# Optimization experiments

Hardware: AMD Instinct MI355X
Metric: run time of the kernel (lower is better)

The kernel has to match this reference:

```python
import jax, jax.numpy as jnp
import numpy as np
from jax import lax

KSIZE = 7
EPS = 1e-10


def _circular_mask(k=KSIZE):
    # faithful to EdgeLoss.cal_mask: inclusive circle, normalized by count
    xs = np.arange(k, dtype=np.float32)
    d2 = (xs[:, None] + 0.5 - k / 2) ** 2 + (xs[None, :] + 0.5 - k / 2) ** 2
    m = (d2 <= ((k - 1) / 2) ** 2).astype(np.float32)
    return jnp.asarray(m / m.sum())


def _gather_logp(prob, target):
    # prob: (B,C,H,W), target: (B,H,W) int -> log prob at target class, (B,1,H,W)
    logpt = jnp.log(prob + EPS)
    return jnp.take_along_axis(logpt, target[:, None, :, :], axis=1)


def _focal0(prob, target):
    # FocalLoss(gamma=0, alpha=None): mean of -log p_t
    return jnp.mean(-_gather_logp(prob, target))


def _dice(prob, target):
    t = target.astype(prob.dtype)          # (B,H,W)
    p = prob[:, 1, :, :]                   # foreground channel
    I = jnp.sum(p * t, axis=(1, 2))
    U = jnp.sum(p + t, axis=(1, 2))
    return 1.0 - jnp.mean(2.0 * I / (U + EPS))


def _edge(prob, target, mask):
    # circular box-filter average of target == unfold+mask sum (zero padding)
    t = target.astype(prob.dtype)[:, None, :, :]  # (B,1,H,W)
    ave = lax.conv_general_dilated(t, mask[None, None, :, :], (1, 1), 'SAME')
    at = jnp.abs(t - ave)                          # edge weight (B,1,H,W)
    lp = _gather_logp(prob, target)                # (B,1,H,W)
    return jnp.mean(-lp * at)


def _calloss(prob, target, sigmas, mask):
    return (_focal0(prob, target) / sigmas[0]
            + _dice(prob, target) / sigmas[1]
            + _edge(prob, target, mask) / sigmas[2])


def setup_inputs() -> dict:
    key = jax.random.key(0)
    k1, k2, k3, k4, k5 = jax.random.split(key, 5)
    N, M, B, C, H, W = 2, 1, 8, 2, 1024, 1024
    predictions = jax.random.normal(k1, (N, B, C, H, W), dtype=jnp.float32)
    Diss = jax.random.uniform(k2, (M, B, C, H, W), dtype=jnp.float32)
    target = jax.random.randint(k3, (B, H, W), 0, 2, dtype=jnp.int32)
    diff = jax.random.normal(k4, (), dtype=jnp.float32)
    sigma = jax.random.uniform(k5, (3,), dtype=jnp.float32, minval=0.5, maxval=1.5)
    return {"predictions": predictions, "Diss": Diss, "target": target,
            "diff": diff, "sigma": sigma}


def reference(predictions, Diss, target, diff, sigma):
    mask = _circular_mask()
    sigmas = sigma * sigma
    loss = jnp.asarray(0.0, dtype=predictions.dtype)
    for i in range(predictions.shape[0]):            # deep-supervision heads
        prob = jax.nn.softmax(predictions[i], axis=1)
        loss = loss + _calloss(prob, target, sigmas, mask)
    for j in range(Diss.shape[0]):                   # already-probabilities
        loss = loss + _calloss(Diss[j], target, sigmas, mask)
    loss = loss + diff                               # len(diff) != 0 branch
    loss = loss + jnp.sum(jnp.log(sigmas)) / 2
    return loss
```

## Files before the change

kernel.cpp:

```cpp
#include <hip/hip_runtime.h>
#include <math.h>

#define BB 8
#define HH 1024
#define WW 1024
#define HW (1024*1024)

#define TW 128
#define TH 16
#define HALO_H (TH+6)
#define TSTRIDE 136
#define NCHUNK (HALO_H*34)
#define NCOPY 64
#define CSTRIDE 64
#define NSLOT 18

__device__ __forceinline__ void pin4(float4& v) {
    asm volatile("" : "+v"(v.x), "+v"(v.y), "+v"(v.z), "+v"(v.w));
}

__global__ __launch_bounds__(256, 4)
void loss_main(const float* __restrict__ pred,
               const float* __restrict__ diss,
               const int*   __restrict__ target,
               double*      __restrict__ acc)
{
    __shared__ __align__(16) unsigned char tile[HALO_H][TSTRIDE];
    __shared__ __align__(16) unsigned char h5[HALO_H][TW];
    __shared__ __align__(16) unsigned char h7[HALO_H][TW];
    __shared__ float red[4][12];

    const int bx = blockIdx.x;
    const int by = blockIdx.y;
    const int b  = blockIdx.z;
    const int x0 = bx * TW, y0 = by * TH;
    const int tid = threadIdx.x;
    const int txx = tid & 31;
    const int ty  = tid >> 5;

    const float* p00 = pred + ((size_t)(0 * BB + b) * 2 + 0) * HW;
    const float* p01 = p00 + HW;
    const float* p10 = pred + ((size_t)(1 * BB + b) * 2 + 0) * HW;
    const float* p11 = p10 + HW;
    const float* q0  = diss + ((size_t)b * 2 + 0) * HW;
    const float* q1  = q0 + HW;

    const int x  = txx * 4;
    const int gx = x0 + x;
    const size_t offA = (size_t)(y0 + ty) * WW + gx;
    const size_t offB = offA + (size_t)8 * WW;

    float4 v00a = *(const float4*)(p00 + offA);
    float4 v01a = *(const float4*)(p01 + offA);
    float4 v10a = *(const float4*)(p10 + offA);
    float4 v11a = *(const float4*)(p11 + offA);
    float4 w0a  = *(const float4*)(q0  + offA);
    float4 w1a  = *(const float4*)(q1  + offA);
    float4 v00b = *(const float4*)(p00 + offB);
    float4 v01b = *(const float4*)(p01 + offB);
    float4 v10b = *(const float4*)(p10 + offB);
    float4 v11b = *(const float4*)(p11 + offB);
    float4 w0b  = *(const float4*)(q0  + offB);
    float4 w1b  = *(const float4*)(q1  + offB);
    __builtin_amdgcn_sched_barrier(0);

    const int* tgt_b = target + (size_t)b * HW;
    int4 iv[3]; int rr[3], mm[3];
    bool act[3], mainp[3], rowin[3];
    #pragma unroll
    for (int i = 0; i < 3; ++i) {
        const int ch = tid + 256 * i;
        const bool a = ch < NCHUNK;
        const int chc = a ? ch : 0;
        const int r = chc / 34;
        const int m = chc - r * 34;
        const int gy  = y0 - 3 + r;
        const int gxb = x0 - 4 + 4 * m;
        const bool ri = (gy >= 0) && (gy < HH);
        const bool fp = a && ri && (gxb >= 0) && (gxb + 3 < WW);
        act[i] = a; rr[i] = r; mm[i] = m; rowin[i] = ri; mainp[i] = fp;
        const int gyc  = ri ? gy  : 0;
        const int gxbc = fp ? gxb : 0;
        iv[i] = *(const int4*)(tgt_b + (size_t)gyc * WW + gxbc);
    }
    #pragma unroll
    for (int i = 0; i < 3; ++i) {
        if (!act[i]) continue;
        unsigned v = 0u;
        if (mainp[i]) {
            v = (unsigned)(iv[i].x & 0xff)
              | ((unsigned)(iv[i].y & 0xff) << 8)
              | ((unsigned)(iv[i].z & 0xff) << 16)
              | ((unsigned)(iv[i].w & 0xff) << 24);
        } else if (rowin[i]) {
            const int gy  = y0 - 3 + rr[i];
            const int gxb = x0 - 4 + 4 * mm[i];
            #pragma unroll
            for (int j = 0; j < 4; ++j) {
                const int gxj = gxb + j;
                if (gxj >= 0 && gxj < WW)
                    v |= (unsigned)(tgt_b[(size_t)gy * WW + gxj] & 0xff) << (8 * j);
            }
        }
        *(unsigned*)&tile[rr[i]][4 * mm[i]] = v;
    }

    pin4(v00a); pin4(v01a); pin4(v10a); pin4(v11a); pin4(w0a); pin4(w1a);
    pin4(v00b); pin4(v01b); pin4(v10b); pin4(v11b); pin4(w0b); pin4(w1b);
    __syncthreads();

    for (int g = tid; g < HALO_H * 32; g += 256) {
        int r  = g >> 5;
        int xg = (g & 31) << 2;
        unsigned c0 = *(const unsigned*)&tile[r][xg];
        unsigned c1 = *(const unsigned*)&tile[r][xg + 4];
        unsigned c2 = *(const unsigned*)&tile[r][xg + 8];
        unsigned A1 = (c0 >> 8)  | (c1 << 24);
        unsigned A2 = (c0 >> 16) | (c1 << 16);
        unsigned A3 = (c0 >> 24) | (c1 << 8);
        unsigned A5 = (c1 >> 8)  | (c2 << 24);
        unsigned A6 = (c1 >> 16) | (c2 << 16);
        unsigned A7 = (c1 >> 24) | (c2 << 8);
        unsigned v5 = A2 + A3 + c1 + A5 + A6;
        unsigned v7 = v5 + A1 + A7;
        *(unsigned*)&h5[r][xg] = v5;
        *(unsigned*)&h7[r][xg] = v7;
    }
    __syncthreads();

    float sf0=0.f, se0=0.f, si0=0.f, sp0=0.f;
    float sf1=0.f, se1=0.f, si1=0.f, sp1=0.f;
    float sf2=0.f, se2=0.f, si2=0.f, sd1=0.f;
    float st = 0.f;

    const unsigned t4a   = *(const unsigned*)&tile[ty + 3][x + 4];
    const unsigned cnt4a = *(const unsigned*)&tile[ty    ][x + 4]
                         + *(const unsigned*)&tile[ty + 6][x + 4]
                         + *(const unsigned*)&h5[ty + 1][x]
                         + *(const unsigned*)&h5[ty + 2][x]
                         + *(const unsigned*)&h7[ty + 3][x]
                         + *(const unsigned*)&h5[ty + 4][x]
                         + *(const unsigned*)&h5[ty + 5][x];
    const unsigned t4b   = *(const unsigned*)&tile[ty + 11][x + 4];
    const unsigned cnt4b = *(const unsigned*)&tile[ty +  8][x + 4]
                         + *(const unsigned*)&tile[ty + 14][x + 4]
                         + *(const unsigned*)&h5[ty +  9][x]
                         + *(const unsigned*)&h5[ty + 10][x]
                         + *(const unsigned*)&h7[ty + 11][x]
                         + *(const unsigned*)&h5[ty + 12][x]
                         + *(const unsigned*)&h5[ty + 13][x];

    auto half = [&](unsigned t4, unsigned cnt4,
                    const float4& v00, const float4& v01,
                    const float4& v10, const float4& v11,
                    const float4& w0,  const float4& w1) {
        #pragma unroll
        for (int j = 0; j < 4; ++j) {
            const unsigned tb = (t4 >> (8 * j)) & 0xffu;
            const float t  = (float)tb;
            const float at = fabsf(t - (float)((cnt4 >> (8 * j)) & 0xffu) * (1.0f / 29.0f));
            st += t;
            {
                float a0 = ((const float*)&v00)[j], a1 = ((const float*)&v01)[j];
                float p1v = __builtin_amdgcn_rcpf(1.0f + __expf(a0 - a1));
                float pt  = (tb != 0u) ? p1v : 1.0f - p1v;
                float lp  = __logf(pt + 1e-10f);
                sf0 -= lp; se0 -= lp * at; si0 += p1v * t; sp0 += p1v;
            }
            {
                float a0 = ((const float*)&v10)[j], a1 = ((const float*)&v11)[j];
                float p1v = __builtin_amdgcn_rcpf(1.0f + __expf(a0 - a1));
                float pt  = (tb != 0u) ? p1v : 1.0f - p1v;
                float lp  = __logf(pt + 1e-10f);
                sf1 -= lp; se1 -= lp * at; si1 += p1v * t; sp1 += p1v;
            }
            {
                float d0 = ((const float*)&w0)[j], d1 = ((const float*)&w1)[j];
                float pt = (tb != 0u) ? d1 : d0;
                float lp = __logf(pt + 1e-10f);
                sf2 -= lp; se2 -= lp * at; si2 += d1 * t; sd1 += d1;
            }
        }
    };
    half(t4a, cnt4a, v00a, v01a, v10a, v11a, w0a, w1a);
    half(t4b, cnt4b, v00b, v01b, v10b, v11b, w0b, w1b);

    float vals[12] = {sf0,se0,si0,sp0+st, sf1,se1,si1,sp1+st, sf2,se2,si2,sd1+st};
    #pragma unroll
    for (int j = 0; j < 12; ++j) {
        float v = vals[j];
        #pragma unroll
        for (int s = 32; s > 0; s >>= 1) v += __shfl_down(v, s, 64);
        vals[j] = v;
    }
    const int wave = tid >> 6;
    const int lane = tid & 63;
    if (lane == 0) {
        #pragma unroll
        for (int j = 0; j < 12; ++j) red[wave][j] = vals[j];
    }
    __syncthreads();
    if (tid < 12) {
        double s = (double)red[0][tid] + (double)red[1][tid]
                 + (double)red[2][tid] + (double)red[3][tid];
        const int img  = tid >> 2;
        const int what = tid & 3;
        int slot;
        if      (what == 0) slot = 0;
        else if (what == 1) slot = 1;
        else if (what == 2) slot = 2 + b;
        else                slot = 10 + b;
        const int copy = (by * 8 + bx) & (NCOPY - 1);
        unsafeAtomicAdd(acc + (size_t)copy * CSTRIDE + (img * NSLOT + slot), s);
    }
}

__global__ __launch_bounds__(256)
void finalize_kernel(const double* __restrict__ acc,
                     const float*  __restrict__ diff,
                     const float*  __restrict__ sigma,
                     float*        __restrict__ out)
{
    __shared__ double ssum[54];
    const int t = threadIdx.x;
    if (t < 216) {
        const int slot_lin = t >> 2;
        const int part     = t & 3;
        const double* p = acc + slot_lin + (size_t)part * 16 * CSTRIDE;
        double s = 0.0;
        #pragma unroll
        for (int j = 0; j < 16; ++j) s += p[(size_t)j * CSTRIDE];
        s += __shfl_down(s, 1, 64);
        s += __shfl_down(s, 2, 64);
        if (part == 0) ssum[slot_lin] = s;
    }
    __syncthreads();
    if (t == 0) {
        const double sig0 = (double)sigma[0] * (double)sigma[0];
        const double sig1 = (double)sigma[1] * (double)sigma[1];
        const double sig2 = (double)sigma[2] * (double)sigma[2];
        const double inv  = 1.0 / (double)((size_t)BB * HW);
        double loss = 0.0;
        for (int i = 0; i < 3; ++i) {
            const double* A = ssum + i * NSLOT;
            double focal = A[0] * inv;
            double edge  = A[1] * inv;
            double dsum  = 0.0;
            for (int b = 0; b < BB; ++b)
                dsum += 2.0 * A[2 + b] / (A[10 + b] + 1e-10);
            double dice = 1.0 - dsum / (double)BB;
            loss += focal / sig0 + dice / sig1 + edge / sig2;
        }
        loss += (double)diff[0];
        loss += 0.5 * (log(sig0) + log(sig1) + log(sig2));
        out[0] = (float)loss;
    }
}

extern "C" void kernel_launch(void* const* d_in, const int* in_sizes, int n_in,
                              void* d_out, int out_size, void* d_ws, size_t ws_size,
                              hipStream_t stream)
{
    const float* pred   = (const float*)d_in[0];
    const float* diss   = (const float*)d_in[1];
    const int*   target = (const int*)  d_in[2];
    const float* diff   = (const float*)d_in[3];
    const float* sigma  = (const float*)d_in[4];
    double* acc = (double*)d_ws;

    (void)hipMemsetAsync(d_ws, 0, (size_t)NCOPY * CSTRIDE * sizeof(double), stream);

    dim3 grid(WW / TW, HH / TH, BB);
    loss_main<<<grid, 256, 0, stream>>>(pred, diss, target, acc);
    finalize_kernel<<<1, 256, 0, stream>>>(acc, diff, sigma, (float*)d_out);
}
```

Measured before the change: 268.5 us.

## Stage prediction and Diss tiles into LDS via async global_load_lds

The six input planes used to be loaded into registers as float4 and pinned so they stayed live. Now they are copied straight into a new 48KB LDS buffer with the global_load_lds builtin, and read back from LDS in the compute phase. The aim is to cut register pressure and let the loads overlap the target-tile build without holding the data in registers. The catch is much more shared memory per block, and the launch-bounds occupancy hint is dropped, so fewer blocks may fit on each CU.

Result: no change. 264.2 us (-1.6%).

```diff
diff --git a/kernel.cpp b/kernel.cpp
--- a/kernel.cpp
+++ b/kernel.cpp
@@ -15,16 +15,19 @@
 #define CSTRIDE 64
 #define NSLOT 18
 
-__device__ __forceinline__ void pin4(float4& v) {
-    asm volatile("" : "+v"(v.x), "+v"(v.y), "+v"(v.z), "+v"(v.w));
-}
-
-__global__ __launch_bounds__(256, 4)
+typedef const __attribute__((address_space(1))) unsigned GU;
+typedef __attribute__((address_space(3))) unsigned LU;
+__device__ __forceinline__ void async16(const float* g, void* lds) {
+    __builtin_amdgcn_global_load_lds((GU*)g, (LU*)lds, 16, 0, 0);
+}
+
+__global__ __launch_bounds__(256)
 void loss_main(const float* __restrict__ pred,
                const float* __restrict__ diss,
                const int*   __restrict__ target,
                double*      __restrict__ acc)
 {
+    __shared__ __align__(16) float planes[6][TH][TW];
     __shared__ __align__(16) unsigned char tile[HALO_H][TSTRIDE];
     __shared__ __align__(16) unsigned char h5[HALO_H][TW];
     __shared__ __align__(16) unsigned char h7[HALO_H][TW];
@@ -37,6 +40,8 @@
     const int tid = threadIdx.x;
     const int txx = tid & 31;
     const int ty  = tid >> 5;
+    const int wv  = tid >> 6;
+    const int ln  = tid & 63;
 
     const float* p00 = pred + ((size_t)(0 * BB + b) * 2 + 0) * HW;
     const float* p01 = p00 + HW;
@@ -45,24 +50,21 @@
     const float* q0  = diss + ((size_t)b * 2 + 0) * HW;
     const float* q1  = q0 + HW;
 
-    const int x  = txx * 4;
-    const int gx = x0 + x;
-    const size_t offA = (size_t)(y0 + ty) * WW + gx;
-    const size_t offB = offA + (size_t)8 * WW;
-
-    float4 v00a = *(const float4*)(p00 + offA);
-    float4 v01a = *(const float4*)(p01 + offA);
-    float4 v10a = *(const float4*)(p10 + offA);
-    float4 v11a = *(const float4*)(p11 + offA);
-    float4 w0a  = *(const float4*)(q0  + offA);
-    float4 w1a  = *(const float4*)(q1  + offA);
-    float4 v00b = *(const float4*)(p00 + offB);
-    float4 v01b = *(const float4*)(p01 + offB);
-    float4 v10b = *(const float4*)(p10 + offB);
-    float4 v11b = *(const float4*)(p11 + offB);
-    float4 w0b  = *(const float4*)(q0  + offB);
-    float4 w1b  = *(const float4*)(q1  + offB);
-    __builtin_amdgcn_sched_barrier(0);
+    {
+        const int r0  = 2 * wv + (ln >> 5);
+        const int r1  = r0 + 8;
+        const int col = (ln & 31) << 2;
+        const size_t g0 = (size_t)(y0 + r0) * WW + x0 + col;
+        const size_t g1 = (size_t)(y0 + r1) * WW + x0 + col;
+        #pragma unroll
+        for (int pl = 0; pl < 6; ++pl) {
+            const float* pp = (pl == 0) ? p00 : (pl == 1) ? p01 :
+                              (pl == 2) ? p10 : (pl == 3) ? p11 :
+                              (pl == 4) ? q0  : q1;
+            async16(pp + g0, &planes[pl][2 * wv][0]);
+            async16(pp + g1, &planes[pl][2 * wv + 8][0]);
+        }
+    }
 
     const int* tgt_b = target + (size_t)b * HW;
     int4 iv[3]; int rr[3], mm[3];
@@ -104,9 +106,6 @@
         }
         *(unsigned*)&tile[rr[i]][4 * mm[i]] = v;
     }
-
-    pin4(v00a); pin4(v01a); pin4(v10a); pin4(v11a); pin4(w0a); pin4(w1a);
-    pin4(v00b); pin4(v01b); pin4(v10b); pin4(v11b); pin4(w0b); pin4(w1b);
     __syncthreads();
 
     for (int g = tid; g < HALO_H * 32; g += 256) {
@@ -133,6 +132,8 @@
     float sf2=0.f, se2=0.f, si2=0.f, sd1=0.f;
     float st = 0.f;
 
+    const int x = txx * 4;
+
     const unsigned t4a   = *(const unsigned*)&tile[ty + 3][x + 4];
     const unsigned cnt4a = *(const unsigned*)&tile[ty    ][x + 4]
                          + *(const unsigned*)&tile[ty + 6][x + 4]
@@ -150,10 +151,13 @@
                          + *(const unsigned*)&h5[ty + 12][x]
                          + *(const unsigned*)&h5[ty + 13][x];
 
-    auto half = [&](unsigned t4, unsigned cnt4,
-                    const float4& v00, const float4& v01,
-                    const float4& v10, const float4& v11,
-                    const float4& w0,  const float4& w1) {
+    auto half = [&](unsigned t4, unsigned cnt4, int row) {
+        const float4 v00 = *(const float4*)&planes[0][row][x];
+        const float4 v01 = *(const float4*)&planes[1][row][x];
+        const float4 v10 = *(const float4*)&planes[2][row][x];
+        const float4 v11 = *(const float4*)&planes[3][row][x];
+        const float4 w0  = *(const float4*)&planes[4][row][x];
+        const float4 w1  = *(const float4*)&planes[5][row][x];
         #pragma unroll
         for (int j = 0; j < 4; ++j) {
             const unsigned tb = (t4 >> (8 * j)) & 0xffu;
@@ -182,8 +186,8 @@
             }
         }
     };
-    half(t4a, cnt4a, v00a, v01a, v10a, v11a, w0a, w1a);
-    half(t4b, cnt4b, v00b, v01b, v10b, v11b, w0b, w1b);
+    half(t4a, cnt4a, ty);
+    half(t4b, cnt4b, ty + 8);
 
     float vals[12] = {sf0,se0,si0,sp0+st, sf1,se1,si1,sp1+st, sf2,se2,si2,sd1+st};
     #pragma unroll
```
